# Performance work log

Measured on AMD Instinct MI355X. Metric: run time of the kernel, lower is better.

Reference implementation:

```python
import jax, jax.numpy as jnp
import numpy as np

TEMPERATURE = 128 ** 0.5  # sqrt(d_k)


def setup_inputs() -> dict:
    key = jax.random.key(0)
    k1, k2, k3 = jax.random.split(key, 3)
    NB, L, DK, DV = 1024, 2048, 128, 128
    q = jax.random.normal(k1, (NB, DK), dtype=jnp.float32)
    k = jax.random.normal(k2, (NB, L, DK), dtype=jnp.float32)
    v = jax.random.normal(k3, (NB, L, DV), dtype=jnp.float32)
    return {"q": q, "k": k, "v": v}


def reference(q, k, v):
    # attn[b, l] = <q[b], k[b, l]> / temperature
    scores = jnp.einsum('bd,bld->bl', q, k) / TEMPERATURE
    attn = jax.nn.softmax(scores, axis=1)  # softmax over l (dim=1)
    # output[b, d] = sum_l attn[b, l] * v[b, l, d]
    output = jnp.einsum('bl,bld->bd', attn, v)
    return (output, attn)
```

## Files before the change

### kernel.cpp

```cpp
#include <hip/hip_runtime.h>
#include <math.h>

#define NB 1024
#define L  2048
#define DK 128
#define DV 128

static constexpr float INV_TEMP = 0.088388347648318447f;

typedef float f32x4 __attribute__((ext_vector_type(4)));

__device__ __forceinline__ f32x4 nt_load4(const float* p) {
    return __builtin_nontemporal_load(reinterpret_cast<const f32x4*>(p));
}

__global__ __launch_bounds__(512, 8)
void mvsdpa_kernel(const float* __restrict__ q,
                   const float* __restrict__ k,
                   const float* __restrict__ v,
                   float* __restrict__ out,
                   float* __restrict__ attn)
{
    const int b    = blockIdx.x;
    const int tid  = threadIdx.x;
    const int wave = tid >> 6;
    const int lane = tid & 63;
    const int half = lane >> 5;
    const int l32  = lane & 31;

    __shared__ float s_scores[L];
    __shared__ float s_red[16];
    __shared__ float s_partial[16][DV];

    const float* qb = q + (size_t)b * DK;
    const float* kb = k + (size_t)b * (size_t)L * DK;
    const float* vb = v + (size_t)b * (size_t)L * DV;

    const f32x4 q4 = *reinterpret_cast<const f32x4*>(qb + l32 * 4);

    const int rbase = wave * 2 + half;

    for (int i = 0; i < L / 32; ++i) {
        const int r0 = i * 32 + rbase;
        const int r1 = r0 + 16;
        const f32x4 k40 = nt_load4(kb + (size_t)r0 * DK + l32 * 4);
        const f32x4 k41 = nt_load4(kb + (size_t)r1 * DK + l32 * 4);
        float d0 = q4.x * k40.x + q4.y * k40.y + q4.z * k40.z + q4.w * k40.w;
        float d1 = q4.x * k41.x + q4.y * k41.y + q4.z * k41.z + q4.w * k41.w;
        #pragma unroll
        for (int m = 1; m < 32; m <<= 1) {
            d0 += __shfl_xor(d0, m);
            d1 += __shfl_xor(d1, m);
        }
        if (l32 == 0) {
            s_scores[r0] = d0 * INV_TEMP;
            s_scores[r1] = d1 * INV_TEMP;
        }
    }

    const f32x4 vp0 = nt_load4(vb + (size_t)(rbase)      * DV + l32 * 4);
    const f32x4 vp1 = nt_load4(vb + (size_t)(rbase + 16) * DV + l32 * 4);
    const f32x4 vp2 = nt_load4(vb + (size_t)(rbase + 32) * DV + l32 * 4);
    const f32x4 vp3 = nt_load4(vb + (size_t)(rbase + 48) * DV + l32 * 4);

    __syncthreads();

    f32x4 sv = *reinterpret_cast<const f32x4*>(&s_scores[tid * 4]);
    float lmax = fmaxf(fmaxf(sv.x, sv.y), fmaxf(sv.z, sv.w));
    #pragma unroll
    for (int m = 1; m < 64; m <<= 1) lmax = fmaxf(lmax, __shfl_xor(lmax, m));

    f32x4 ev;
    ev.x = __expf(sv.x - lmax);
    ev.y = __expf(sv.y - lmax);
    ev.z = __expf(sv.z - lmax);
    ev.w = __expf(sv.w - lmax);
    float lsum = ev.x + ev.y + ev.z + ev.w;
    #pragma unroll
    for (int m = 1; m < 64; m <<= 1) lsum += __shfl_xor(lsum, m);

    if (lane == 0) { s_red[wave] = lmax; s_red[8 + wave] = lsum; }
    __syncthreads();

    float gmax = s_red[0];
    #pragma unroll
    for (int w = 1; w < 8; ++w) gmax = fmaxf(gmax, s_red[w]);
    float gsum = 0.f;
    #pragma unroll
    for (int w = 0; w < 8; ++w) gsum += s_red[8 + w] * __expf(s_red[w] - gmax);
    const float scale = __expf(lmax - gmax) / gsum;

    sv.x = ev.x * scale; sv.y = ev.y * scale; sv.z = ev.z * scale; sv.w = ev.w * scale;
    *reinterpret_cast<f32x4*>(&s_scores[tid * 4]) = sv;
    *reinterpret_cast<f32x4*>(attn + (size_t)b * L + tid * 4) = sv;
    __syncthreads();

    f32x4 acc;
    {
        const float p0 = s_scores[rbase];
        const float p1 = s_scores[rbase + 16];
        const float p2 = s_scores[rbase + 32];
        const float p3 = s_scores[rbase + 48];
        acc.x = p0 * vp0.x + p1 * vp1.x + p2 * vp2.x + p3 * vp3.x;
        acc.y = p0 * vp0.y + p1 * vp1.y + p2 * vp2.y + p3 * vp3.y;
        acc.z = p0 * vp0.z + p1 * vp1.z + p2 * vp2.z + p3 * vp3.z;
        acc.w = p0 * vp0.w + p1 * vp1.w + p2 * vp2.w + p3 * vp3.w;
    }
    for (int i = 2; i < L / 32; ++i) {
        const int r0 = i * 32 + rbase;
        const int r1 = r0 + 16;
        const f32x4 v0 = nt_load4(vb + (size_t)r0 * DV + l32 * 4);
        const f32x4 v1 = nt_load4(vb + (size_t)r1 * DV + l32 * 4);
        const float p0 = s_scores[r0];
        const float p1 = s_scores[r1];
        acc.x += p0 * v0.x + p1 * v1.x;
        acc.y += p0 * v0.y + p1 * v1.y;
        acc.z += p0 * v0.z + p1 * v1.z;
        acc.w += p0 * v0.w + p1 * v1.w;
    }
    *reinterpret_cast<f32x4*>(&s_partial[wave * 2 + half][l32 * 4]) = acc;
    __syncthreads();
    if (tid < DV) {
        float s = 0.f;
        #pragma unroll
        for (int w = 0; w < 16; ++w) s += s_partial[w][tid];
        out[(size_t)b * DV + tid] = s;
    }
}

extern "C" void kernel_launch(void* const* d_in, const int* in_sizes, int n_in,
                              void* d_out, int out_size, void* d_ws, size_t ws_size,
                              hipStream_t stream) {
    const float* q = (const float*)d_in[0];
    const float* k = (const float*)d_in[1];
    const float* v = (const float*)d_in[2];
    float* out  = (float*)d_out;
    float* attn = (float*)d_out + (size_t)NB * DV;
    mvsdpa_kernel<<<NB, 512, 0, stream>>>(q, k, v, out, attn);
}
```

Before: 318.1 us.

## Give each wave a contiguous chunk and defer softmax normalization across waves

Each wave now owns a contiguous chunk of L, computes its own local max and exp-sum and unnormalized probabilities, and runs its V accumulation before any block-wide barrier. The cross-wave rescaling factor is applied at the end to both the accumulator and the attn output, which removes two __syncthreads between the score and PV phases. Intra-wave LDS ordering relies on explicit s_waitcnt instead of barriers, and the attn and out stores are now nontemporal. The risk lies in whether wave-local LDS visibility is correct without barriers, and in the different access pattern per wave (contiguous rows instead of interleaved).

```diff
diff --git a/kernel.cpp b/kernel.cpp
--- a/kernel.cpp
+++ b/kernel.cpp
@@ -5,6 +5,7 @@
 #define L  2048
 #define DK 128
 #define DV 128
+#define CHUNK (L / 8)
 
 static constexpr float INV_TEMP = 0.088388347648318447f;
 
@@ -12,6 +13,9 @@
 
 __device__ __forceinline__ f32x4 nt_load4(const float* p) {
     return __builtin_nontemporal_load(reinterpret_cast<const f32x4*>(p));
+}
+__device__ __forceinline__ void nt_store4(float* p, f32x4 x) {
+    __builtin_nontemporal_store(x, reinterpret_cast<f32x4*>(p));
 }
 
 __global__ __launch_bounds__(512, 8)
@@ -38,11 +42,12 @@
 
     const f32x4 q4 = *reinterpret_cast<const f32x4*>(qb + l32 * 4);
 
-    const int rbase = wave * 2 + half;
+    const int c0 = wave * CHUNK;
 
-    for (int i = 0; i < L / 32; ++i) {
-        const int r0 = i * 32 + rbase;
-        const int r1 = r0 + 16;
+    float lmax = -INFINITY;
+    for (int i = 0; i < CHUNK / 4; ++i) {
+        const int r0 = c0 + i * 4 + half * 2;
+        const int r1 = r0 + 1;
         const f32x4 k40 = nt_load4(kb + (size_t)r0 * DK + l32 * 4);
         const f32x4 k41 = nt_load4(kb + (size_t)r1 * DK + l32 * 4);
         float d0 = q4.x * k40.x + q4.y * k40.y + q4.z * k40.z + q4.w * k40.w;
@@ -52,63 +57,47 @@
             d0 += __shfl_xor(d0, m);
             d1 += __shfl_xor(d1, m);
         }
-        if (l32 == 0) {
-            s_scores[r0] = d0 * INV_TEMP;
-            s_scores[r1] = d1 * INV_TEMP;
-        }
+        d0 *= INV_TEMP;
+        d1 *= INV_TEMP;
+        lmax = fmaxf(lmax, fmaxf(d0, d1));
+        if (l32 == 0) { s_scores[r0] = d0; s_scores[r1] = d1; }
     }
+    lmax = fmaxf(lmax, __shfl_xor(lmax, 32));
 
-    const f32x4 vp0 = nt_load4(vb + (size_t)(rbase)      * DV + l32 * 4);
-    const f32x4 vp1 = nt_load4(vb + (size_t)(rbase + 16) * DV + l32 * 4);
-    const f32x4 vp2 = nt_load4(vb + (size_t)(rbase + 32) * DV + l32 * 4);
-    const f32x4 vp3 = nt_load4(vb + (size_t)(rbase + 48) * DV + l32 * 4);
+    const int pr0 = c0 + half * 2;
+    const f32x4 vp0 = nt_load4(vb + (size_t)(pr0)     * DV + l32 * 4);
+    const f32x4 vp1 = nt_load4(vb + (size_t)(pr0 + 1) * DV + l32 * 4);
+    const f32x4 vp2 = nt_load4(vb + (size_t)(pr0 + 4) * DV + l32 * 4);
+    const f32x4 vp3 = nt_load4(vb + (size_t)(pr0 + 5) * DV + l32 * 4);
 
-    __syncthreads();
-
-    f32x4 sv = *reinterpret_cast<const f32x4*>(&s_scores[tid * 4]);
-    float lmax = fmaxf(fmaxf(sv.x, sv.y), fmaxf(sv.z, sv.w));
-    #pragma unroll
-    for (int m = 1; m < 64; m <<= 1) lmax = fmaxf(lmax, __shfl_xor(lmax, m));
-
-    f32x4 ev;
-    ev.x = __expf(sv.x - lmax);
-    ev.y = __expf(sv.y - lmax);
-    ev.z = __expf(sv.z - lmax);
-    ev.w = __expf(sv.w - lmax);
-    float lsum = ev.x + ev.y + ev.z + ev.w;
+    asm volatile("s_waitcnt lgkmcnt(0)" ::: "memory");
+    const f32x4 sv = *reinterpret_cast<const f32x4*>(&s_scores[c0 + lane * 4]);
+    f32x4 pw;
+    pw.x = __expf(sv.x - lmax);
+    pw.y = __expf(sv.y - lmax);
+    pw.z = __expf(sv.z - lmax);
+    pw.w = __expf(sv.w - lmax);
+    float lsum = pw.x + pw.y + pw.z + pw.w;
     #pragma unroll
     for (int m = 1; m < 64; m <<= 1) lsum += __shfl_xor(lsum, m);
-
+    *reinterpret_cast<f32x4*>(&s_scores[c0 + lane * 4]) = pw;
     if (lane == 0) { s_red[wave] = lmax; s_red[8 + wave] = lsum; }
-    __syncthreads();
-
-    float gmax = s_red[0];
-    #pragma unroll
-    for (int w = 1; w < 8; ++w) gmax = fmaxf(gmax, s_red[w]);
-    float gsum = 0.f;
-    #pragma unroll
-    for (int w = 0; w < 8; ++w) gsum += s_red[8 + w] * __expf(s_red[w] - gmax);
-    const float scale = __expf(lmax - gmax) / gsum;
-
-    sv.x = ev.x * scale; sv.y = ev.y * scale; sv.z = ev.z * scale; sv.w = ev.w * scale;
-    *reinterpret_cast<f32x4*>(&s_scores[tid * 4]) = sv;
-    *reinterpret_cast<f32x4*>(attn + (size_t)b * L + tid * 4) = sv;
-    __syncthreads();
+    asm volatile("s_waitcnt lgkmcnt(0)" ::: "memory");
 
     f32x4 acc;
     {
-        const float p0 = s_scores[rbase];
-        const float p1 = s_scores[rbase + 16];
-        const float p2 = s_scores[rbase + 32];
-        const float p3 = s_scores[rbase + 48];
+        const float p0 = s_scores[pr0];
+        const float p1 = s_scores[pr0 + 1];
+        const float p2 = s_scores[pr0 + 4];
+        const float p3 = s_scores[pr0 + 5];
         acc.x = p0 * vp0.x + p1 * vp1.x + p2 * vp2.x + p3 * vp3.x;
         acc.y = p0 * vp0.y + p1 * vp1.y + p2 * vp2.y + p3 * vp3.y;
         acc.z = p0 * vp0.z + p1 * vp1.z + p2 * vp2.z + p3 * vp3.z;
         acc.w = p0 * vp0.w + p1 * vp1.w + p2 * vp2.w + p3 * vp3.w;
     }
-    for (int i = 2; i < L / 32; ++i) {
-        const int r0 = i * 32 + rbase;
-        const int r1 = r0 + 16;
+    for (int i = 2; i < CHUNK / 4; ++i) {
+        const int r0 = c0 + i * 4 + half * 2;
+        const int r1 = r0 + 1;
         const f32x4 v0 = nt_load4(vb + (size_t)r0 * DV + l32 * 4);
         const f32x4 v1 = nt_load4(vb + (size_t)r1 * DV + l32 * 4);
         const float p0 = s_scores[r0];
@@ -118,13 +107,27 @@
         acc.z += p0 * v0.z + p1 * v1.z;
         acc.w += p0 * v0.w + p1 * v1.w;
     }
+
+    __syncthreads();
+
+    float gmax = s_red[0];
+    #pragma unroll
+    for (int w = 1; w < 8; ++w) gmax = fmaxf(gmax, s_red[w]);
+    float gsum = 0.f;
+    #pragma unroll
+    for (int w = 0; w < 8; ++w) gsum += s_red[8 + w] * __expf(s_red[w] - gmax);
+    const float factor = __expf(lmax - gmax) / gsum;
+
+    nt_store4(attn + (size_t)b * L + c0 + lane * 4, pw * factor);
+
+    acc *= factor;
     *reinterpret_cast<f32x4*>(&s_partial[wave * 2 + half][l32 * 4]) = acc;
     __syncthreads();
     if (tid < DV) {
         float s = 0.f;
         #pragma unroll
         for (int w = 0; w < 16; ++w) s += s_partial[w][tid];
-        out[(size_t)b * DV + tid] = s;
+        __builtin_nontemporal_store(s, out + (size_t)b * DV + tid);
     }
 }
 
```

Result: slower. 339.5 us (+6.7%).
